# Kernel tuning notes

Measured on AMD Instinct MI355X. Metric: run time of the kernel, lower is better.

The kernel has to match this reference:

```python
import jax, jax.numpy as jnp
import numpy as np

B, S, D, NL, H, KV, F, V, R = 4, 1024, 2048, 2, 16, 4, 8192, 32000, 16
HD = D // H                      # 128, Llama-3 head dim
LORA_SCALE = 32.0 / 16.0         # alpha / r
ROPE_THETA = 500000.0
EPS = 1e-5


def _rope_tables(seq_len, hd):
    inv = 1.0 / (ROPE_THETA ** (jnp.arange(0, hd, 2, dtype=jnp.float32) / hd))
    freqs = jnp.arange(seq_len, dtype=jnp.float32)[:, None] * inv[None, :]   # [S, hd/2]
    emb = jnp.concatenate([freqs, freqs], axis=-1)                           # [S, hd]
    return jnp.cos(emb), jnp.sin(emb)


def _apply_rope(x, cos, sin):
    # x: [B, S, nh, HD]; LLaMA rotate_half convention
    h = x.shape[-1] // 2
    rot = jnp.concatenate([-x[..., h:], x[..., :h]], axis=-1)
    return x * cos[None, :, None, :] + rot * sin[None, :, None, :]


def _rmsnorm(x, w):
    return x * jax.lax.rsqrt(jnp.mean(x * x, axis=-1, keepdims=True) + EPS) * w


def _forward(embed, wq, wk, wv, wo, laq, lbq, lav, lbv, wg, wu, wd, n1, n2, nf,
             input_ids, attention_mask):
    b, s = input_ids.shape
    cos, sin = _rope_tables(s, HD)
    amask = attention_mask.astype(bool)
    # causal AND key-padding mask: [B, 1, S, S]
    mask = jnp.tril(jnp.ones((s, s), bool))[None, None] & amask[:, None, None, :]
    x = embed[input_ids]                                   # [B, S, D]
    for l in range(NL):
        h = _rmsnorm(x, n1[l])
        # base projection + LoRA adapter (q and v only, as in target_modules)
        q = h @ wq[l] + ((h @ laq[l].T) @ lbq[l].T) * LORA_SCALE
        k = h @ wk[l]
        v = h @ wv[l] + ((h @ lav[l].T) @ lbv[l].T) * LORA_SCALE
        q = _apply_rope(q.reshape(b, s, H, HD), cos, sin)
        k = _apply_rope(k.reshape(b, s, KV, HD), cos, sin)
        v = v.reshape(b, s, KV, HD)
        k = jnp.repeat(k, H // KV, axis=2)                 # GQA expand
        v = jnp.repeat(v, H // KV, axis=2)
        scores = jnp.einsum('bqhd,bkhd->bhqk', q, k) / jnp.float32(np.sqrt(HD))
        scores = jnp.where(mask, scores, jnp.float32(-1e9))
        attn = jax.nn.softmax(scores, axis=-1)
        o = jnp.einsum('bhqk,bkhd->bqhd', attn, v).reshape(b, s, D)
        x = x + o @ wo[l]
        h2 = _rmsnorm(x, n2[l])
        x = x + (jax.nn.silu(h2 @ wg[l]) * (h2 @ wu[l])) @ wd[l]
    h = _rmsnorm(x, nf)                                    # final norm -> last_hidden_state
    m = attention_mask.astype(jnp.float32)[..., None]
    return (h * m).sum(axis=1) / jnp.clip(m.sum(axis=1), 1e-9)   # masked mean pool [B, D]


def setup_inputs() -> dict:
    key = jax.random.key(0)
    ks = jax.random.split(key, 14)
    sd = 0.02
    nrm = lambda k, shape: sd * jax.random.normal(k, shape, dtype=jnp.float32)
    return {
        'embed': nrm(ks[0], (V, D)),
        'wq': nrm(ks[1], (NL, D, D)),
        'wk': nrm(ks[2], (NL, D, KV * HD)),
        'wv': nrm(ks[3], (NL, D, KV * HD)),
        'wo': nrm(ks[4], (NL, D, D)),
        'laq': nrm(ks[5], (NL, R, D)),
        'lbq': nrm(ks[6], (NL, D, R)),
        'lav': nrm(ks[7], (NL, R, D)),
        'lbv': nrm(ks[8], (NL, KV * HD, R)),
        'wg': nrm(ks[9], (NL, D, F)),
        'wu': nrm(ks[10], (NL, D, F)),
        'wd': nrm(ks[11], (NL, F, D)),
        'n1': jnp.ones((NL, D), jnp.float32),
        'n2': jnp.ones((NL, D), jnp.float32),
        'nf': jnp.ones((D,), jnp.float32),
        'input_ids': jax.random.randint(ks[12], (B, S), 0, V, dtype=jnp.int32),
        'attention_mask': jnp.ones((B, S), jnp.int32),
    }


def reference(embed, wq, wk, wv, wo, laq, lbq, lav, lbv, wg, wu, wd, n1, n2, nf,
              input_ids, attention_mask):
    return _forward(embed, wq, wk, wv, wo, laq, lbq, lav, lbv, wg, wu, wd,
                    n1, n2, nf, input_ids, attention_mask)
```

## Files before the change

kernel.cpp:

```cpp
#include <hip/hip_runtime.h>
#include <math.h>

#define B_  4
#define S_  1024
#define D_  2048
#define NL_ 2
#define H_  16
#define KV_ 4
#define F_  8192
#define R_  16
#define HD_ 128
#define BS_ (B_*S_)
#define QBLK 64
#define KBLK 64

typedef unsigned short u16;
typedef __attribute__((ext_vector_type(8))) __bf16 bf16x8;
typedef __attribute__((ext_vector_type(4))) float  f32x4;

__device__ __forceinline__ u16 f2bf(float f) {
    unsigned x = __float_as_uint(f);
    unsigned r = (x + 0x7fffu + ((x >> 16) & 1u)) >> 16;
    return (u16)r;
}
__device__ __forceinline__ float bf2f(u16 u) {
    return __uint_as_float(((unsigned)u) << 16);
}

__device__ __forceinline__ void gload16(const void* g, void* l) {
    __builtin_amdgcn_global_load_lds((const __attribute__((address_space(1))) void*)g,
                                     (__attribute__((address_space(3))) void*)l, 16, 0, 0);
}

__global__ void embed_kernel(const float* __restrict__ embed,
                             const int* __restrict__ ids,
                             float* __restrict__ x) {
    int tok = blockIdx.x;
    int id  = ids[tok];
    const float4* src = (const float4*)(embed + (size_t)id * D_);
    float4*       dst = (float4*)(x + (size_t)tok * D_);
    for (int i = threadIdx.x; i < D_/4; i += blockDim.x) dst[i] = src[i];
}

template<int OUTBF>
__global__ __launch_bounds__(256) void rmsnorm_kernel(const float* __restrict__ x,
                                                      const float* __restrict__ w,
                                                      void* __restrict__ out) {
    int row = blockIdx.x;
    const float4* xr = (const float4*)(x + (size_t)row * D_);
    float ss = 0.f;
    for (int i = threadIdx.x; i < D_/4; i += 256) {
        float4 v = xr[i];
        ss += v.x*v.x + v.y*v.y + v.z*v.z + v.w*v.w;
    }
    __shared__ float red[4];
    for (int off = 32; off; off >>= 1) ss += __shfl_down(ss, off);
    if ((threadIdx.x & 63) == 0) red[threadIdx.x >> 6] = ss;
    __syncthreads();
    float tot = red[0] + red[1] + red[2] + red[3];
    float scale = rsqrtf(tot / (float)D_ + 1e-5f);
    const float4* w4 = (const float4*)w;
    for (int i = threadIdx.x; i < D_/4; i += 256) {
        float4 v = xr[i], g = w4[i];
        float a = v.x*scale*g.x, b = v.y*scale*g.y, c = v.z*scale*g.z, d = v.w*scale*g.w;
        if (OUTBF) {
            ushort4 o; o.x = f2bf(a); o.y = f2bf(b); o.z = f2bf(c); o.w = f2bf(d);
            ((ushort4*)((u16*)out + (size_t)row * D_))[i] = o;
        } else {
            float4 o; o.x = a; o.y = b; o.z = c; o.w = d;
            ((float4*)((float*)out + (size_t)row * D_))[i] = o;
        }
    }
}

__global__ __launch_bounds__(256) void convt_kernel(const float* __restrict__ in,
                                                    u16* __restrict__ outT,
                                                    int K, int N) {
    __shared__ float tile[32][33];
    int k0 = blockIdx.y * 32, n0 = blockIdx.x * 32;
    int t = threadIdx.x;
    int r = t >> 3, c4 = (t & 7) * 4;
    float4 v = *(const float4*)(in + (size_t)(k0 + r) * N + n0 + c4);
    tile[r][c4] = v.x; tile[r][c4+1] = v.y; tile[r][c4+2] = v.z; tile[r][c4+3] = v.w;
    __syncthreads();
    int n = t >> 3, kc = (t & 7) * 4;
    ushort4 o;
    o.x = f2bf(tile[kc][n]);   o.y = f2bf(tile[kc+1][n]);
    o.z = f2bf(tile[kc+2][n]); o.w = f2bf(tile[kc+3][n]);
    *(ushort4*)(outT + (size_t)(n0 + n) * K + k0 + kc) = o;
}

template<int ACC>
__global__ __launch_bounds__(256) void gemm_bt(const u16* __restrict__ A,
                                               const u16* __restrict__ Bt,
                                               float* __restrict__ C,
                                               int N, int K) {
    __shared__ __align__(16) u16 As[128*64];
    __shared__ __align__(16) u16 Bs[128*64];
    int tid = threadIdx.x, lane = tid & 63;
    int wid = tid >> 6, wm = wid >> 1, wn = wid & 1;
    int m0 = blockIdx.y * 128, n0 = blockIdx.x * 128;
    const u16* Ab = A  + (size_t)m0 * K;
    const u16* Bb = Bt + (size_t)n0 * K;
    f32x4 acc[4][4] = {};
    for (int k0 = 0; k0 < K; k0 += 64) {
        #pragma unroll
        for (int qq = 0; qq < 4; qq++) {
            int u = qq * 256 + tid;
            int row = u >> 3, cu = u & 7, scu = cu ^ (row & 7);
            size_t goff = (size_t)row * K + k0 + scu * 8;
            gload16(Ab + goff, (char*)As + u * 16);
            gload16(Bb + goff, (char*)Bs + u * 16);
        }
        __syncthreads();
        #pragma unroll
        for (int kk = 0; kk < 2; kk++) {
            int cu = kk * 4 + (lane >> 4);
            bf16x8 af[4], bfr[4];
            #pragma unroll
            for (int i = 0; i < 4; i++) {
                int ar = wm * 64 + i * 16 + (lane & 15);
                af[i]  = *(const bf16x8*)((const char*)As + (((ar << 3) | (cu ^ (ar & 7))) << 4));
                int br = wn * 64 + i * 16 + (lane & 15);
                bfr[i] = *(const bf16x8*)((const char*)Bs + (((br << 3) | (cu ^ (br & 7))) << 4));
            }
            #pragma unroll
            for (int i = 0; i < 4; i++)
                #pragma unroll
                for (int j = 0; j < 4; j++)
                    acc[i][j] = __builtin_amdgcn_mfma_f32_16x16x32_bf16(af[i], bfr[j], acc[i][j], 0, 0, 0);
        }
        __syncthreads();
    }
    int r0 = (lane >> 4) * 4, c0 = lane & 15;
    #pragma unroll
    for (int i = 0; i < 4; i++)
        #pragma unroll
        for (int j = 0; j < 4; j++) {
            int row = m0 + wm * 64 + i * 16 + r0;
            int col = n0 + wn * 64 + j * 16 + c0;
            float* cp = C + (size_t)row * N + col;
            #pragma unroll
            for (int r = 0; r < 4; r++) {
                if (ACC) cp[(size_t)r * N] += acc[i][j][r];
                else     cp[(size_t)r * N] = acc[i][j][r];
            }
        }
}

__global__ __launch_bounds__(256) void gemm_gateup_bt(const u16* __restrict__ A,
                                                      const u16* __restrict__ Gt,
                                                      const u16* __restrict__ Ut,
                                                      u16* __restrict__ act,
                                                      int N, int K) {
    __shared__ __align__(16) u16 As[128*64];
    __shared__ __align__(16) u16 Gs[64*64];
    __shared__ __align__(16) u16 Us[64*64];
    int tid = threadIdx.x, lane = tid & 63;
    int wid = tid >> 6, wm = wid >> 1, wn = wid & 1;
    int m0 = blockIdx.y * 128, n0 = blockIdx.x * 64;
    const u16* Ab = A  + (size_t)m0 * K;
    const u16* Gb = Gt + (size_t)n0 * K;
    const u16* Ub = Ut + (size_t)n0 * K;
    f32x4 ag[4][2] = {}, au[4][2] = {};
    for (int k0 = 0; k0 < K; k0 += 64) {
        #pragma unroll
        for (int qq = 0; qq < 4; qq++) {
            int u = qq * 256 + tid;
            int row = u >> 3, cu = u & 7, scu = cu ^ (row & 7);
            gload16(Ab + (size_t)row * K + k0 + scu * 8, (char*)As + u * 16);
        }
        #pragma unroll
        for (int qq = 0; qq < 2; qq++) {
            int u = qq * 256 + tid;
            int row = u >> 3, cu = u & 7, scu = cu ^ (row & 7);
            size_t goff = (size_t)row * K + k0 + scu * 8;
            gload16(Gb + goff, (char*)Gs + u * 16);
            gload16(Ub + goff, (char*)Us + u * 16);
        }
        __syncthreads();
        #pragma unroll
        for (int kk = 0; kk < 2; kk++) {
            int cu = kk * 4 + (lane >> 4);
            bf16x8 af[4], gf[2], uf[2];
            #pragma unroll
            for (int i = 0; i < 4; i++) {
                int ar = wm * 64 + i * 16 + (lane & 15);
                af[i] = *(const bf16x8*)((const char*)As + (((ar << 3) | (cu ^ (ar & 7))) << 4));
            }
            #pragma unroll
            for (int j = 0; j < 2; j++) {
                int br = wn * 32 + j * 16 + (lane & 15);
                int off = ((br << 3) | (cu ^ (br & 7))) << 4;
                gf[j] = *(const bf16x8*)((const char*)Gs + off);
                uf[j] = *(const bf16x8*)((const char*)Us + off);
            }
            #pragma unroll
            for (int i = 0; i < 4; i++)
                #pragma unroll
                for (int j = 0; j < 2; j++) {
                    ag[i][j] = __builtin_amdgcn_mfma_f32_16x16x32_bf16(af[i], gf[j], ag[i][j], 0, 0, 0);
                    au[i][j] = __builtin_amdgcn_mfma_f32_16x16x32_bf16(af[i], uf[j], au[i][j], 0, 0, 0);
                }
        }
        __syncthreads();
    }
    int r0 = (lane >> 4) * 4, c0 = lane & 15;
    #pragma unroll
    for (int i = 0; i < 4; i++)
        #pragma unroll
        for (int j = 0; j < 2; j++) {
            int col = n0 + wn * 32 + j * 16 + c0;
            #pragma unroll
            for (int r = 0; r < 4; r++) {
                int row = m0 + wm * 64 + i * 16 + r0 + r;
                float g = ag[i][j][r], u = au[i][j][r];
                float s = g / (1.f + __expf(-g));
                act[(size_t)row * N + col] = f2bf(s * u);
            }
        }
}

__global__ __launch_bounds__(256) void lora_a_kernel(const u16* __restrict__ h,
                                                     const float* __restrict__ la,
                                                     float* __restrict__ t16) {
    int r = threadIdx.x >> 4;
    int c = threadIdx.x & 15;
    int row = blockIdx.x * 16 + r;
    const ushort4* hr = (const ushort4*)(h + (size_t)row * D_);
    const float4* lr = (const float4*)(la + (size_t)c * D_);
    float acc = 0.f;
    #pragma unroll 4
    for (int i = 0; i < D_/4; i++) {
        ushort4 a = hr[i]; float4 b = lr[i];
        acc += bf2f(a.x)*b.x + bf2f(a.y)*b.y + bf2f(a.z)*b.z + bf2f(a.w)*b.w;
    }
    t16[(size_t)row * R_ + c] = acc;
}

__global__ __launch_bounds__(256) void lora_b_kernel(const float* __restrict__ t16,
                                                     const float* __restrict__ lb,
                                                     float* __restrict__ out, int N) {
    int row = blockIdx.x;
    __shared__ float ts[R_];
    if (threadIdx.x < R_) ts[threadIdx.x] = t16[(size_t)row * R_ + threadIdx.x];
    __syncthreads();
    for (int d = threadIdx.x; d < N; d += 256) {
        const float4* lbr = (const float4*)(lb + (size_t)d * R_);
        float acc = 0.f;
        #pragma unroll
        for (int r4 = 0; r4 < 4; r4++) {
            float4 v = lbr[r4];
            acc += v.x*ts[r4*4] + v.y*ts[r4*4+1] + v.z*ts[r4*4+2] + v.w*ts[r4*4+3];
        }
        out[(size_t)row * N + d] += 2.0f * acc;
    }
}

__global__ void qconv_rope(const float* __restrict__ q, u16* __restrict__ Qc) {
    int tok = blockIdx.x, h = blockIdx.y, t = threadIdx.x;
    int b = tok >> 10, s = tok & (S_ - 1);
    float inv = __expf(-(float)t * (13.122363377404328f / 64.0f));
    float f = (float)s * inv;
    float c = __cosf(f), si = __sinf(f);
    const float* src = q + ((size_t)tok * H_ + h) * HD_;
    float x0 = src[t], x1 = src[t + 64];
    u16* dst = Qc + (((size_t)(b * H_ + h)) * S_ + s) * HD_;
    dst[t]      = f2bf(x0 * c - x1 * si);
    dst[t + 64] = f2bf(x1 * c + x0 * si);
}

__global__ void kconv_rope(const float* __restrict__ k, u16* __restrict__ Kc) {
    int tok = blockIdx.x, h = blockIdx.y, t = threadIdx.x;
    int b = tok >> 10, s = tok & (S_ - 1);
    float inv = __expf(-(float)t * (13.122363377404328f / 64.0f));
    float f = (float)s * inv;
    float c = __cosf(f), si = __sinf(f);
    const float* src = k + ((size_t)tok * KV_ + h) * HD_;
    float x0 = src[t], x1 = src[t + 64];
    u16* dst = Kc + (((size_t)(b * KV_ + h)) * S_ + s) * HD_;
    dst[t]      = f2bf(x0 * c - x1 * si);
    dst[t + 64] = f2bf(x1 * c + x0 * si);
}

__global__ __launch_bounds__(256) void vconv_t(const float* __restrict__ vb,
                                               u16* __restrict__ Vt) {
    __shared__ float tile[32][33];
    int s0 = blockIdx.x * 32, d0 = blockIdx.y * 32;
    int bk = blockIdx.z;
    int b = bk >> 2, kvh = bk & 3;
    int t = threadIdx.x;
    int r = t >> 3, c4 = (t & 7) * 4;
    float4 v = *(const float4*)(vb + (((size_t)(b * S_ + s0 + r)) * KV_ + kvh) * HD_ + d0 + c4);
    tile[r][c4] = v.x; tile[r][c4+1] = v.y; tile[r][c4+2] = v.z; tile[r][c4+3] = v.w;
    __syncthreads();
    int dr = t >> 3, s4 = (t & 7) * 4;
    ushort4 o;
    o.x = f2bf(tile[s4][dr]);   o.y = f2bf(tile[s4+1][dr]);
    o.z = f2bf(tile[s4+2][dr]); o.w = f2bf(tile[s4+3][dr]);
    *(ushort4*)(Vt + (((size_t)(b * KV_ + kvh)) * HD_ + d0 + dr) * S_ + s0 + s4) = o;
}

__global__ __launch_bounds__(256) void flash_attn(const u16* __restrict__ Qc,
                                                  const u16* __restrict__ Kc,
                                                  const u16* __restrict__ Vt,
                                                  const int* __restrict__ am,
                                                  u16* __restrict__ o) {
    __shared__ __align__(16) u16 Ks[64 * 128];
    __shared__ __align__(16) u16 Vs[128 * 64];
    __shared__ __align__(16) u16 Ps[4][16][72];
    __shared__ int am_s[KBLK];
    int qt = blockIdx.x, h = blockIdx.y, b = blockIdx.z;
    int kvh = h >> 2;
    int tid = threadIdx.x, lane = tid & 63, w = tid >> 6;
    int g = lane >> 4, li = lane & 15;

    bf16x8 qf[4];
    const u16* qb = Qc + (((size_t)(b * H_ + h)) * S_ + qt * QBLK + w * 16 + li) * HD_;
    #pragma unroll
    for (int dd = 0; dd < 4; dd++) qf[dd] = *(const bf16x8*)(qb + dd * 32 + g * 8);

    float m_r[4], l_r[4];
    f32x4 oacc[8];
    #pragma unroll
    for (int r = 0; r < 4; r++) { m_r[r] = -1e30f; l_r[r] = 0.f; }
    #pragma unroll
    for (int d = 0; d < 8; d++) oacc[d] = (f32x4){0.f, 0.f, 0.f, 0.f};

    const u16* Kg = Kc + ((size_t)(b * KV_ + kvh)) * S_ * HD_;
    const u16* Vg = Vt + ((size_t)(b * KV_ + kvh)) * HD_ * S_;
    int qg0 = qt * QBLK + w * 16 + g * 4;

    for (int kvt = 0; kvt <= qt; kvt++) {
        int kv0 = kvt * KBLK;
        #pragma unroll
        for (int qq = 0; qq < 4; qq++) {
            int u = qq * 256 + tid;
            int row = u >> 4, p = u & 15;
            gload16(Kg + (size_t)(kv0 + row) * HD_ + (p ^ (row & 7)) * 8, (char*)Ks + u * 16);
        }
        #pragma unroll
        for (int qq = 0; qq < 4; qq++) {
            int u = qq * 256 + tid;
            int row = u >> 3, p = u & 7;
            gload16(Vg + (size_t)row * S_ + kv0 + (p ^ (row & 7)) * 8, (char*)Vs + u * 16);
        }
        if (tid < KBLK) am_s[tid] = am[b * S_ + kv0 + tid];
        __syncthreads();

        float ps[4][4];
        #pragma unroll
        for (int kt = 0; kt < 4; kt++) {
            f32x4 sa = (f32x4){0.f, 0.f, 0.f, 0.f};
            int row = kt * 16 + li;
            #pragma unroll
            for (int dd = 0; dd < 4; dd++) {
                int c = dd * 4 + g;
                bf16x8 kf = *(const bf16x8*)((const char*)Ks + ((row * 16 + (c ^ (row & 7))) << 4));
                sa = __builtin_amdgcn_mfma_f32_16x16x32_bf16(qf[dd], kf, sa, 0, 0, 0);
            }
            int kcol = kv0 + kt * 16 + li;
            int amok = am_s[kt * 16 + li];
            #pragma unroll
            for (int r = 0; r < 4; r++) {
                float s = sa[r] * 0.08838834764831845f;
                ps[kt][r] = (amok && kcol <= qg0 + r) ? s : -1e9f;
            }
        }

        float rmax[4], rsum[4], scl[4];
        #pragma unroll
        for (int r = 0; r < 4; r++)
            rmax[r] = fmaxf(fmaxf(ps[0][r], ps[1][r]), fmaxf(ps[2][r], ps[3][r]));
        #pragma unroll
        for (int msk = 1; msk < 16; msk <<= 1)
            #pragma unroll
            for (int r = 0; r < 4; r++) rmax[r] = fmaxf(rmax[r], __shfl_xor(rmax[r], msk));
        #pragma unroll
        for (int r = 0; r < 4; r++) {
            float mn = fmaxf(m_r[r], rmax[r]);
            scl[r] = __expf(m_r[r] - mn);
            m_r[r] = mn;
            rsum[r] = 0.f;
        }
        #pragma unroll
        for (int kt = 0; kt < 4; kt++)
            #pragma unroll
            for (int r = 0; r < 4; r++) {
                float p = __expf(ps[kt][r] - m_r[r]);
                ps[kt][r] = p;
                rsum[r] += p;
            }
        #pragma unroll
        for (int msk = 1; msk < 16; msk <<= 1)
            #pragma unroll
            for (int r = 0; r < 4; r++) rsum[r] += __shfl_xor(rsum[r], msk);
        #pragma unroll
        for (int r = 0; r < 4; r++) l_r[r] = l_r[r] * scl[r] + rsum[r];
        #pragma unroll
        for (int d = 0; d < 8; d++)
            #pragma unroll
            for (int r = 0; r < 4; r++) oacc[d][r] *= scl[r];

        #pragma unroll
        for (int kt = 0; kt < 4; kt++)
            #pragma unroll
            for (int r = 0; r < 4; r++)
                Ps[w][g * 4 + r][kt * 16 + li] = f2bf(ps[kt][r]);
        __syncthreads();

        bf16x8 pf[2];
        #pragma unroll
        for (int ks = 0; ks < 2; ks++)
            pf[ks] = *(const bf16x8*)&Ps[w][li][ks * 32 + g * 8];
        #pragma unroll
        for (int dblk = 0; dblk < 8; dblk++) {
            int row = dblk * 16 + li;
            #pragma unroll
            for (int ks = 0; ks < 2; ks++) {
                int c = ks * 4 + g;
                bf16x8 vf = *(const bf16x8*)((const char*)Vs + ((row * 8 + (c ^ (row & 7))) << 4));
                oacc[dblk] = __builtin_amdgcn_mfma_f32_16x16x32_bf16(pf[ks], vf, oacc[dblk], 0, 0, 0);
            }
        }
        __syncthreads();
    }

    float invl[4];
    #pragma unroll
    for (int r = 0; r < 4; r++) invl[r] = 1.f / l_r[r];
    #pragma unroll
    for (int dblk = 0; dblk < 8; dblk++)
        #pragma unroll
        for (int r = 0; r < 4; r++) {
            int qrow = qg0 + r;
            o[(((size_t)b * S_ + qrow) * H_ + h) * HD_ + dblk * 16 + li] =
                f2bf(oacc[dblk][r] * invl[r]);
        }
}

__global__ __launch_bounds__(256) void pool_kernel(const float* __restrict__ h,
                                                   const int* __restrict__ am,
                                                   float* __restrict__ out) {
    int b = blockIdx.y;
    int d = blockIdx.x * 256 + threadIdx.x;
    float acc = 0.f, ms = 0.f;
    for (int s = 0; s < S_; s++) {
        float mm = (float)am[b * S_ + s];
        ms  += mm;
        acc += mm * h[((size_t)b * S_ + s) * D_ + d];
    }
    out[(size_t)b * D_ + d] = acc / fmaxf(ms, 1e-9f);
}

extern "C" void kernel_launch(void* const* d_in, const int* in_sizes, int n_in,
                              void* d_out, int out_size, void* d_ws, size_t ws_size,
                              hipStream_t stream) {
    const float* embed = (const float*)d_in[0];
    const float* wq    = (const float*)d_in[1];
    const float* wk    = (const float*)d_in[2];
    const float* wv    = (const float*)d_in[3];
    const float* wo    = (const float*)d_in[4];
    const float* laq   = (const float*)d_in[5];
    const float* lbq   = (const float*)d_in[6];
    const float* lav   = (const float*)d_in[7];
    const float* lbv   = (const float*)d_in[8];
    const float* wg    = (const float*)d_in[9];
    const float* wu    = (const float*)d_in[10];
    const float* wd    = (const float*)d_in[11];
    const float* n1    = (const float*)d_in[12];
    const float* n2    = (const float*)d_in[13];
    const float* nf    = (const float*)d_in[14];
    const int*   ids   = (const int*)d_in[15];
    const int*   am    = (const int*)d_in[16];
    float* out = (float*)d_out;

    char* base = (char*)d_ws;
    float* x   = (float*)base;
    u16*   hbf = (u16*)(base + 33554432);
    u16*   obf = (u16*)(base + 50331648);
    char*  Rg  = base + 67108864;
    float* q   = (float*)Rg;
    float* kb  = (float*)(Rg + 33554432);
    float* vb  = (float*)(Rg + 41943040);
    u16*   act = (u16*)Rg;
    float* hf  = (float*)Rg;
    float* t16 = (float*)(base + 134217728);
    u16*   wT0 = (u16*)(base + 134479872);
    u16*   wT1 = (u16*)(base + 168034304);
    u16*   Qc  = (u16*)(base + 201588736);
    u16*   Kc  = (u16*)(base + 218365952);
    u16*   Vtb = (u16*)(base + 222560256);

    embed_kernel<<<BS_, 256, 0, stream>>>(embed, ids, x);

    for (int l = 0; l < NL_; l++) {
        const float* wql = wq + (size_t)l * D_ * D_;
        const float* wkl = wk + (size_t)l * D_ * (KV_*HD_);
        const float* wvl = wv + (size_t)l * D_ * (KV_*HD_);
        const float* wol = wo + (size_t)l * D_ * D_;
        const float* wgl = wg + (size_t)l * D_ * F_;
        const float* wul = wu + (size_t)l * D_ * F_;
        const float* wdl = wd + (size_t)l * F_ * D_;

        rmsnorm_kernel<1><<<BS_, 256, 0, stream>>>(x, n1 + (size_t)l * D_, hbf);

        convt_kernel<<<dim3(D_/32, D_/32), 256, 0, stream>>>(wql, wT0, D_, D_);
        gemm_bt<0><<<dim3(D_/128, BS_/128), 256, 0, stream>>>(hbf, wT0, q, D_, D_);
        lora_a_kernel<<<BS_/16, 256, 0, stream>>>(hbf, laq + (size_t)l * R_ * D_, t16);
        lora_b_kernel<<<BS_, 256, 0, stream>>>(t16, lbq + (size_t)l * D_ * R_, q, D_);

        convt_kernel<<<dim3((KV_*HD_)/32, D_/32), 256, 0, stream>>>(wkl, wT0, D_, KV_*HD_);
        gemm_bt<0><<<dim3((KV_*HD_)/128, BS_/128), 256, 0, stream>>>(hbf, wT0, kb, KV_*HD_, D_);
        convt_kernel<<<dim3((KV_*HD_)/32, D_/32), 256, 0, stream>>>(wvl, wT0, D_, KV_*HD_);
        gemm_bt<0><<<dim3((KV_*HD_)/128, BS_/128), 256, 0, stream>>>(hbf, wT0, vb, KV_*HD_, D_);
        lora_a_kernel<<<BS_/16, 256, 0, stream>>>(hbf, lav + (size_t)l * R_ * D_, t16);
        lora_b_kernel<<<BS_, 256, 0, stream>>>(t16, lbv + (size_t)l * (KV_*HD_) * R_, vb, KV_*HD_);

        qconv_rope<<<dim3(BS_, H_),  64, 0, stream>>>(q,  Qc);
        kconv_rope<<<dim3(BS_, KV_), 64, 0, stream>>>(kb, Kc);
        vconv_t<<<dim3(S_/32, HD_/32, B_*KV_), 256, 0, stream>>>(vb, Vtb);

        flash_attn<<<dim3(S_/QBLK, H_, B_), 256, 0, stream>>>(Qc, Kc, Vtb, am, obf);

        convt_kernel<<<dim3(D_/32, D_/32), 256, 0, stream>>>(wol, wT0, D_, D_);
        gemm_bt<1><<<dim3(D_/128, BS_/128), 256, 0, stream>>>(obf, wT0, x, D_, D_);

        rmsnorm_kernel<1><<<BS_, 256, 0, stream>>>(x, n2 + (size_t)l * D_, hbf);
        convt_kernel<<<dim3(F_/32, D_/32), 256, 0, stream>>>(wgl, wT0, D_, F_);
        convt_kernel<<<dim3(F_/32, D_/32), 256, 0, stream>>>(wul, wT1, D_, F_);
        gemm_gateup_bt<<<dim3(F_/64, BS_/128), 256, 0, stream>>>(hbf, wT0, wT1, act, F_, D_);
        convt_kernel<<<dim3(D_/32, F_/32), 256, 0, stream>>>(wdl, wT0, F_, D_);
        gemm_bt<1><<<dim3(D_/128, BS_/128), 256, 0, stream>>>(act, wT0, x, D_, F_);
    }

    rmsnorm_kernel<0><<<BS_, 256, 0, stream>>>(x, nf, hf);
    pool_kernel<<<dim3(D_/256, B_), 256, 0, stream>>>(hf, am, out);
}
```

Measured before the change: 2.190 ms.

## Share KV tiles across GQA heads in flash attention and swizzle GEMM blocks across XCDs

Flash attention now launches one 512-thread block per (32-query tile, KV head, batch), with 8 waves covering the 4 query heads that share a KV head. Each K/V tile is loaded once into LDS and reused by all four heads instead of being reloaded per head. Waves whose query rows lie entirely before a KV tile skip that tile's compute, and the wave-private Ps sync is dropped. GEMM kernels also remap block IDs so neighbouring tiles land on the same XCD for better L2 locality, at the cost of a larger block and more LDS pressure in attention.

```diff
diff --git a/kernel.cpp b/kernel.cpp
--- a/kernel.cpp
+++ b/kernel.cpp
@@ -11,7 +11,7 @@
 #define R_  16
 #define HD_ 128
 #define BS_ (B_*S_)
-#define QBLK 64
+#define QT2 32
 #define KBLK 64
 
 typedef unsigned short u16;
@@ -30,6 +30,17 @@
 __device__ __forceinline__ void gload16(const void* g, void* l) {
     __builtin_amdgcn_global_load_lds((const __attribute__((address_space(1))) void*)g,
                                      (__attribute__((address_space(3))) void*)l, 16, 0, 0);
+}
+
+__device__ __forceinline__ void xcd_swz(int& bx, int& by) {
+    int gx = gridDim.x;
+    int n  = gx * gridDim.y;
+    if ((n & 7) == 0) {
+        int id  = by * gx + bx;
+        int cpx = n >> 3;
+        int s   = (id & 7) * cpx + (id >> 3);
+        bx = s % gx; by = s / gx;
+    }
 }
 
 __global__ void embed_kernel(const float* __restrict__ embed,
@@ -99,7 +110,9 @@
     __shared__ __align__(16) u16 Bs[128*64];
     int tid = threadIdx.x, lane = tid & 63;
     int wid = tid >> 6, wm = wid >> 1, wn = wid & 1;
-    int m0 = blockIdx.y * 128, n0 = blockIdx.x * 128;
+    int bx = blockIdx.x, by = blockIdx.y;
+    xcd_swz(bx, by);
+    int m0 = by * 128, n0 = bx * 128;
     const u16* Ab = A  + (size_t)m0 * K;
     const u16* Bb = Bt + (size_t)n0 * K;
     f32x4 acc[4][4] = {};
@@ -158,7 +171,9 @@
     __shared__ __align__(16) u16 Us[64*64];
     int tid = threadIdx.x, lane = tid & 63;
     int wid = tid >> 6, wm = wid >> 1, wn = wid & 1;
-    int m0 = blockIdx.y * 128, n0 = blockIdx.x * 64;
+    int bx = blockIdx.x, by = blockIdx.y;
+    xcd_swz(bx, by);
+    int m0 = by * 128, n0 = bx * 64;
     const u16* Ab = A  + (size_t)m0 * K;
     const u16* Gb = Gt + (size_t)n0 * K;
     const u16* Ub = Ut + (size_t)n0 * K;
@@ -301,22 +316,23 @@
     *(ushort4*)(Vt + (((size_t)(b * KV_ + kvh)) * HD_ + d0 + dr) * S_ + s0 + s4) = o;
 }
 
-__global__ __launch_bounds__(256) void flash_attn(const u16* __restrict__ Qc,
+__global__ __launch_bounds__(512) void flash_attn(const u16* __restrict__ Qc,
                                                   const u16* __restrict__ Kc,
                                                   const u16* __restrict__ Vt,
                                                   const int* __restrict__ am,
                                                   u16* __restrict__ o) {
     __shared__ __align__(16) u16 Ks[64 * 128];
     __shared__ __align__(16) u16 Vs[128 * 64];
-    __shared__ __align__(16) u16 Ps[4][16][72];
+    __shared__ __align__(16) u16 Ps[8][16][72];
     __shared__ int am_s[KBLK];
-    int qt = blockIdx.x, h = blockIdx.y, b = blockIdx.z;
-    int kvh = h >> 2;
+    int qt = blockIdx.x, kvh = blockIdx.y, b = blockIdx.z;
     int tid = threadIdx.x, lane = tid & 63, w = tid >> 6;
     int g = lane >> 4, li = lane & 15;
+    int h = kvh * 4 + (w & 3);
+    int qrow0 = qt * QT2 + (w >> 2) * 16;
 
     bf16x8 qf[4];
-    const u16* qb = Qc + (((size_t)(b * H_ + h)) * S_ + qt * QBLK + w * 16 + li) * HD_;
+    const u16* qb = Qc + (((size_t)(b * H_ + h)) * S_ + qrow0 + li) * HD_;
     #pragma unroll
     for (int dd = 0; dd < 4; dd++) qf[dd] = *(const bf16x8*)(qb + dd * 32 + g * 8);
 
@@ -329,98 +345,96 @@
 
     const u16* Kg = Kc + ((size_t)(b * KV_ + kvh)) * S_ * HD_;
     const u16* Vg = Vt + ((size_t)(b * KV_ + kvh)) * HD_ * S_;
-    int qg0 = qt * QBLK + w * 16 + g * 4;
-
-    for (int kvt = 0; kvt <= qt; kvt++) {
+    int qg0 = qrow0 + g * 4;
+    int nkv = (qt * QT2 + QT2 - 1) >> 6;
+
+    for (int kvt = 0; kvt <= nkv; kvt++) {
         int kv0 = kvt * KBLK;
         #pragma unroll
-        for (int qq = 0; qq < 4; qq++) {
-            int u = qq * 256 + tid;
-            int row = u >> 4, p = u & 15;
-            gload16(Kg + (size_t)(kv0 + row) * HD_ + (p ^ (row & 7)) * 8, (char*)Ks + u * 16);
-        }
-        #pragma unroll
-        for (int qq = 0; qq < 4; qq++) {
-            int u = qq * 256 + tid;
-            int row = u >> 3, p = u & 7;
-            gload16(Vg + (size_t)row * S_ + kv0 + (p ^ (row & 7)) * 8, (char*)Vs + u * 16);
+        for (int qq = 0; qq < 2; qq++) {
+            int u = qq * 512 + tid;
+            int krow = u >> 4, p = u & 15;
+            gload16(Kg + (size_t)(kv0 + krow) * HD_ + (p ^ (krow & 7)) * 8, (char*)Ks + u * 16);
+            int vrow = u >> 3, pv = u & 7;
+            gload16(Vg + (size_t)vrow * S_ + kv0 + (pv ^ (vrow & 7)) * 8, (char*)Vs + u * 16);
         }
         if (tid < KBLK) am_s[tid] = am[b * S_ + kv0 + tid];
         __syncthreads();
 
-        float ps[4][4];
-        #pragma unroll
-        for (int kt = 0; kt < 4; kt++) {
-            f32x4 sa = (f32x4){0.f, 0.f, 0.f, 0.f};
-            int row = kt * 16 + li;
-            #pragma unroll
-            for (int dd = 0; dd < 4; dd++) {
-                int c = dd * 4 + g;
-                bf16x8 kf = *(const bf16x8*)((const char*)Ks + ((row * 16 + (c ^ (row & 7))) << 4));
-                sa = __builtin_amdgcn_mfma_f32_16x16x32_bf16(qf[dd], kf, sa, 0, 0, 0);
-            }
-            int kcol = kv0 + kt * 16 + li;
-            int amok = am_s[kt * 16 + li];
+        if (kv0 <= qrow0 + 15) {
+            float ps[4][4];
+            #pragma unroll
+            for (int kt = 0; kt < 4; kt++) {
+                f32x4 sa = (f32x4){0.f, 0.f, 0.f, 0.f};
+                int row = kt * 16 + li;
+                #pragma unroll
+                for (int dd = 0; dd < 4; dd++) {
+                    int c = dd * 4 + g;
+                    bf16x8 kf = *(const bf16x8*)((const char*)Ks + ((row * 16 + (c ^ (row & 7))) << 4));
+                    sa = __builtin_amdgcn_mfma_f32_16x16x32_bf16(qf[dd], kf, sa, 0, 0, 0);
+                }
+                int kcol = kv0 + kt * 16 + li;
+                int amok = am_s[kt * 16 + li];
+                #pragma unroll
+                for (int r = 0; r < 4; r++) {
+                    float s = sa[r] * 0.08838834764831845f;
+                    ps[kt][r] = (amok && kcol <= qg0 + r) ? s : -1e9f;
+                }
+            }
+
+            float rmax[4], rsum[4], scl[4];
+            #pragma unroll
+            for (int r = 0; r < 4; r++)
+                rmax[r] = fmaxf(fmaxf(ps[0][r], ps[1][r]), fmaxf(ps[2][r], ps[3][r]));
+            #pragma unroll
+            for (int msk = 1; msk < 16; msk <<= 1)
+                #pragma unroll
+                for (int r = 0; r < 4; r++) rmax[r] = fmaxf(rmax[r], __shfl_xor(rmax[r], msk));
             #pragma unroll
             for (int r = 0; r < 4; r++) {
-                float s = sa[r] * 0.08838834764831845f;
-                ps[kt][r] = (amok && kcol <= qg0 + r) ? s : -1e9f;
-            }
-        }
-
-        float rmax[4], rsum[4], scl[4];
-        #pragma unroll
-        for (int r = 0; r < 4; r++)
-            rmax[r] = fmaxf(fmaxf(ps[0][r], ps[1][r]), fmaxf(ps[2][r], ps[3][r]));
-        #pragma unroll
-        for (int msk = 1; msk < 16; msk <<= 1)
-            #pragma unroll
-            for (int r = 0; r < 4; r++) rmax[r] = fmaxf(rmax[r], __shfl_xor(rmax[r], msk));
-        #pragma unroll
-        for (int r = 0; r < 4; r++) {
-            float mn = fmaxf(m_r[r], rmax[r]);
-            scl[r] = __expf(m_r[r] - mn);
-            m_r[r] = mn;
-            rsum[r] = 0.f;
-        }
-        #pragma unroll
-        for (int kt = 0; kt < 4; kt++)
-            #pragma unroll
-            for (int r = 0; r < 4; r++) {
-                float p = __expf(ps[kt][r] - m_r[r]);
-                ps[kt][r] = p;
-                rsum[r] += p;
-            }
-        #pragma unroll
-        for (int msk = 1; msk < 16; msk <<= 1)
-            #pragma unroll
-            for (int r = 0; r < 4; r++) rsum[r] += __shfl_xor(rsum[r], msk);
-        #pragma unroll
-        for (int r = 0; r < 4; r++) l_r[r] = l_r[r] * scl[r] + rsum[r];
-        #pragma unroll
-        for (int d = 0; d < 8; d++)
-            #pragma unroll
-            for (int r = 0; r < 4; r++) oacc[d][r] *= scl[r];
-
-        #pragma unroll
-        for (int kt = 0; kt < 4; kt++)
-            #pragma unroll
-            for (int r = 0; r < 4; r++)
-                Ps[w][g * 4 + r][kt * 16 + li] = f2bf(ps[kt][r]);
-        __syncthreads();
-
-        bf16x8 pf[2];
-        #pragma unroll
-        for (int ks = 0; ks < 2; ks++)
-            pf[ks] = *(const bf16x8*)&Ps[w][li][ks * 32 + g * 8];
-        #pragma unroll
-        for (int dblk = 0; dblk < 8; dblk++) {
-            int row = dblk * 16 + li;
-            #pragma unroll
-            for (int ks = 0; ks < 2; ks++) {
-                int c = ks * 4 + g;
-                bf16x8 vf = *(const bf16x8*)((const char*)Vs + ((row * 8 + (c ^ (row & 7))) << 4));
-                oacc[dblk] = __builtin_amdgcn_mfma_f32_16x16x32_bf16(pf[ks], vf, oacc[dblk], 0, 0, 0);
+                float mn = fmaxf(m_r[r], rmax[r]);
+                scl[r] = __expf(m_r[r] - mn);
+                m_r[r] = mn;
+                rsum[r] = 0.f;
+            }
+            #pragma unroll
+            for (int kt = 0; kt < 4; kt++)
+                #pragma unroll
+                for (int r = 0; r < 4; r++) {
+                    float p = __expf(ps[kt][r] - m_r[r]);
+                    ps[kt][r] = p;
+                    rsum[r] += p;
+                }
+            #pragma unroll
+            for (int msk = 1; msk < 16; msk <<= 1)
+                #pragma unroll
+                for (int r = 0; r < 4; r++) rsum[r] += __shfl_xor(rsum[r], msk);
+            #pragma unroll
+            for (int r = 0; r < 4; r++) l_r[r] = l_r[r] * scl[r] + rsum[r];
+            #pragma unroll
+            for (int d = 0; d < 8; d++)
+                #pragma unroll
+                for (int r = 0; r < 4; r++) oacc[d][r] *= scl[r];
+
+            #pragma unroll
+            for (int kt = 0; kt < 4; kt++)
+                #pragma unroll
+                for (int r = 0; r < 4; r++)
+                    Ps[w][g * 4 + r][kt * 16 + li] = f2bf(ps[kt][r]);
+            bf16x8 pf[2];
+            #pragma unroll
+            for (int ks = 0; ks < 2; ks++)
+                pf[ks] = *(const bf16x8*)&Ps[w][li][ks * 32 + g * 8];
+
+            #pragma unroll
+            for (int dblk = 0; dblk < 8; dblk++) {
+                int row = dblk * 16 + li;
+                #pragma unroll
+                for (int ks = 0; ks < 2; ks++) {
+                    int c = ks * 4 + g;
+                    bf16x8 vf = *(const bf16x8*)((const char*)Vs + ((row * 8 + (c ^ (row & 7))) << 4));
+                    oacc[dblk] = __builtin_amdgcn_mfma_f32_16x16x32_bf16(pf[ks], vf, oacc[dblk], 0, 0, 0);
+                }
             }
         }
         __syncthreads();
@@ -521,7 +535,7 @@
         kconv_rope<<<dim3(BS_, KV_), 64, 0, stream>>>(kb, Kc);
         vconv_t<<<dim3(S_/32, HD_/32, B_*KV_), 256, 0, stream>>>(vb, Vtb);
 
-        flash_attn<<<dim3(S_/QBLK, H_, B_), 256, 0, stream>>>(Qc, Kc, Vtb, am, obf);
+        flash_attn<<<dim3(S_/QT2, KV_, B_), 512, 0, stream>>>(Qc, Kc, Vtb, am, obf);
 
         convt_kernel<<<dim3(D_/32, D_/32), 256, 0, stream>>>(wol, wT0, D_, D_);
         gemm_bt<1><<<dim3(D_/128, BS_/128), 256, 0, stream>>>(obf, wT0, x, D_, D_);
```

Measured after the change: 2.220 ms. No clear change (+1.4%).
